# Optimization experiments

Hardware: AMD Instinct MI355X
Metric: run time of the kernel (lower is better)

The kernel has to match this reference:

```python
import jax, jax.numpy as jnp
import numpy as np

T = 2048
N = 4096
DT = 0.01
V_RESET = 1.0
ALPHA = 0.01
MAX_SPIKES = 128


def setup_inputs() -> dict:
    key = jax.random.key(0)
    ks = jax.random.split(key, 8)
    ts = jnp.arange(T, dtype=jnp.float32) * DT
    input_current = jax.random.normal(ks[0], (T, N), dtype=jnp.float32)
    # _build_w: uniform(minval=0.5) fully-connected weight matrix
    w = jax.random.uniform(ks[1], (N, N), dtype=jnp.float32, minval=0.5, maxval=1.0)
    # _build_initial: uniform(maxval=0.1)
    v0 = jax.random.uniform(ks[2], (N,), dtype=jnp.float32, maxval=0.1)
    i0 = jax.random.uniform(ks[3], (N,), dtype=jnp.float32, maxval=0.1)
    mu = jax.random.uniform(ks[4], (2,), dtype=jnp.float32, minval=0.5, maxval=1.0)
    # uniforms for initial s and for post-spike s resampling (s = log(u) - alpha)
    s0_u = jax.random.uniform(ks[5], (N,), dtype=jnp.float32)
    resample_u = jax.random.uniform(ks[6], (T, N), dtype=jnp.float32)
    return {"ts": ts, "input_current": input_current, "w": w, "v0": v0,
            "i0": i0, "mu": mu, "s0_u": s0_u, "resample_u": resample_u,
            "max_spikes": MAX_SPIKES}


def reference(ts, input_current, w, v0, i0, mu, s0_u, resample_u, max_spikes):
    """Event-driven spiking net: Euler integration of the drift vf with
    spike events when s crosses 0, followed by the masked per-neuron jump
    transition (_inner_trans_fn) using the firing neuron's weight row.
    Returns trajectory ys [T, N, 3] (v, i, s per neuron)."""
    dt = ts[1] - ts[0]
    eps = jnp.float32(1e-12)
    # s0 = log(uniform) - alpha  (always negative; drifts up at rate intensity(v))
    s0 = jnp.log(s0_u + eps) - ALPHA
    y0 = jnp.stack([v0, i0, s0], axis=-1)  # [N, 3]
    mu1, mu2 = mu[0], mu[1]

    def step(carry, xs):
        y, nsp = carry
        inp_t, ru_t = xs
        v, i, s = y[:, 0], y[:, 1], y[:, 2]
        # drift_vf (Euler step)
        v_n = v + dt * (mu1 * (i - v) + mu1 * inp_t)
        i_n = i + dt * (-mu2 * i)
        s_n = s + dt * jax.nn.sigmoid(v)  # intensity_fn(v)
        # event detection: cond_fn = s; event when s reaches 0
        ev = s_n >= 0.0  # [N] event mask
        fire = jnp.any(ev) & (nsp < max_spikes)
        idx = jnp.argmax(ev)  # event_idx = argmax over event mask
        w_row = w[idx]  # weights from firing neuron to all neurons
        # _inner_trans_fn: spiking neurons reset v and resample s;
        # non-spiking neurons receive current injection w[idx][j]
        v_t = jnp.where(ev, v_n - V_RESET, v_n)
        i_t = jnp.where(ev, i_n, i_n + w_row)
        s_t = jnp.where(ev, jnp.log(ru_t + eps) - ALPHA, s_n)
        y_fire = jnp.stack([v_t, i_t, s_t], axis=-1)
        y_free = jnp.stack([v_n, i_n, s_n], axis=-1)
        y_out = jnp.where(fire, y_fire, y_free)
        nsp = nsp + fire.astype(jnp.int32)
        return (y_out, nsp), y_out

    (_, _), ys = jax.lax.scan(step, (y0, jnp.int32(0)),
                              (input_current, resample_u))
    return ys
```

## Files before the change

### kernel.cpp

```cpp
#include <hip/hip_runtime.h>
#include <stddef.h>

#define TT 2048
#define NN 4096
#define LSEG 64
#define NSEG (TT / LSEG)
#define NBLK 16
#define TPA 64
#define NPT 4
#define TPB 256
#define WCAP 256
#define MAXU 0xFFFFFFFFu
#define NOFIRE 0xFFFFFFFEu

__global__ __launch_bounds__(TPA) void phaseA1(
    const float* __restrict__ ts, const float* __restrict__ inp,
    const float* __restrict__ w, const float* __restrict__ v0,
    const float* __restrict__ i0, const float* __restrict__ mu,
    const float* __restrict__ s0u, const float* __restrict__ ru,
    const int* __restrict__ mx, unsigned int* __restrict__ hdr,
    unsigned int* __restrict__ slots, unsigned int* __restrict__ fireT,
    unsigned int* __restrict__ fireIdx)
{
#pragma clang fp contract(off)
  const int tid = threadIdx.x;
  const int blk = blockIdx.x;
  const int idx4 = blk * TPA + tid;
  const int n0 = idx4 * NPT;
  const float dt = ts[1] - ts[0];
  const float mu1 = mu[0], mu2 = mu[1];
  const int maxs = mx[0];

  const float4* inp4 = (const float4*)inp;
  const float4* ru4  = (const float4*)ru;
  const float4* w4   = (const float4*)w;

  float4 a4;
  a4 = ((const float4*)v0)[idx4];  float v[NPT]    = {a4.x, a4.y, a4.z, a4.w};
  a4 = ((const float4*)i0)[idx4];  float i_nw[NPT] = {a4.x, a4.y, a4.z, a4.w};
  a4 = ((const float4*)s0u)[idx4];
  float s[NPT] = {logf(a4.x + 1e-12f) - 0.01f, logf(a4.y + 1e-12f) - 0.01f,
                  logf(a4.z + 1e-12f) - 0.01f, logf(a4.w + 1e-12f) - 0.01f};

  float snP[NPT] = {0.f, 0.f, 0.f, 0.f};
  bool  evP[NPT] = {false, false, false, false};
  bool  aw[NPT]  = {false, false, false, false};
  float wvP[NPT] = {0.f, 0.f, 0.f, 0.f};
  float4 inp_cur = make_float4(0.f,0.f,0.f,0.f);
  float4 ru_cur  = make_float4(0.f,0.f,0.f,0.f);
  int nsp = 0;
  int t_stop = TT;
  bool pubPrev = false;

  for (int t = 0;; ++t) {
    bool  fire2 = false;
    bool  awN[NPT] = {false, false, false, false};
    float wN[NPT]  = {0.f, 0.f, 0.f, 0.f};

    if (t >= 2) {
      unsigned int gm2 = NOFIRE;
      if (pubPrev) {
        const unsigned int* row = &slots[(size_t)(t - 2) * NBLK];
        unsigned int x = MAXU;
        long g = 0;
        for (;;) {
          x = __hip_atomic_load(&row[tid & (NBLK - 1)], __ATOMIC_RELAXED,
                                __HIP_MEMORY_SCOPE_AGENT);
          if (__ballot(x != MAXU) == ~0ULL) break;
          if (++g > (1L << 20)) break;
        }
        gm2 = x;
#pragma unroll
        for (int off = 1; off < NBLK; off <<= 1) {
          unsigned int o = (unsigned int)__shfl_xor((int)gm2, off, 64);
          gm2 = gm2 < o ? gm2 : o;
        }
      }
      fire2 = (gm2 < (unsigned int)NN) && (nsp < maxs);
      if (fire2) {
        if (blk == 0 && tid == 0 && nsp < WCAP) {
          fireT[nsp] = (unsigned int)(t - 2);
          fireIdx[nsp] = gm2;
        }
        float4 wr = w4[(size_t)gm2 * (NN / 4) + idx4];
        wN[0] = wr.x; wN[1] = wr.y; wN[2] = wr.z; wN[3] = wr.w;
#pragma unroll
        for (int k = 0; k < NPT; ++k) awN[k] = !evP[k];
        nsp += 1;
        if (nsp >= maxs) {
          t_stop = ((t - 1 + LSEG - 1) / LSEG) * LSEG;
          if (t_stop > TT) t_stop = TT;
          break;
        }
      }
      if (t - 1 == TT) { t_stop = TT; break; }
    }

    if (t >= 2) {
      float iv[NPT] = {inp_cur.x, inp_cur.y, inp_cur.z, inp_cur.w};
      float rv[NPT] = {ru_cur.x,  ru_cur.y,  ru_cur.z,  ru_cur.w};
#pragma unroll
      for (int k = 0; k < NPT; ++k) {
        float ifull = aw[k] ? (i_nw[k] + wvP[k]) : i_nw[k];
        float vn  = v[k] + dt * (mu1 * (ifull - v[k]) + mu1 * iv[k]);
        float in_ = ifull + dt * (-mu2 * ifull);
        if (evP[k] && fire2) {
          v[k] = vn - 1.0f;
          s[k] = logf(rv[k] + 1e-12f) - 0.01f;
        } else {
          v[k] = vn; s[k] = snP[k];
        }
        i_nw[k] = in_;
      }
    }

    bool pubNow = false;
    bool evN[NPT] = {false, false, false, false};
    if (t >= 1) {
      unsigned int m = NOFIRE;
#pragma unroll
      for (int k = 0; k < NPT; ++k) {
        float sig = 1.0f / (1.0f + expf(-v[k]));
        float sn = s[k] + dt * sig;
        snP[k] = sn;
        bool e = sn >= 0.0f;
        evN[k] = e;
        unsigned int c = e ? (unsigned int)(n0 + k) : NOFIRE;
        m = m < c ? m : c;
      }
#pragma unroll
      for (int off = 1; off < 64; off <<= 1) {
        unsigned int o = (unsigned int)__shfl_xor((int)m, off, 64);
        m = m < o ? m : o;
      }
      if (tid == 0)
        __hip_atomic_store(&slots[(size_t)(t - 1) * NBLK + blk], m,
                           __ATOMIC_RELAXED, __HIP_MEMORY_SCOPE_AGENT);
      pubNow = true;
    }

    float4 inw = make_float4(0.f,0.f,0.f,0.f);
    float4 rnw = make_float4(0.f,0.f,0.f,0.f);
    if (t >= 1 && t - 1 < TT) {
      inw = inp4[(size_t)(t - 1) * (NN / 4) + idx4];
      rnw = ru4[(size_t)(t - 1) * (NN / 4) + idx4];
    }

#pragma unroll
    for (int k = 0; k < NPT; ++k) {
      evP[k] = evN[k]; aw[k] = awN[k]; wvP[k] = wN[k];
    }
    inp_cur = inw; ru_cur = rnw;
    pubPrev = pubNow;
  }

  if (blk == 0 && tid == 0) {
    hdr[0] = (unsigned int)t_stop;
    hdr[1] = (unsigned int)nsp;
  }
}

__global__ __launch_bounds__(TPA) void phaseA2(
    const float* __restrict__ ts, const float* __restrict__ inp,
    const float* __restrict__ w, const float* __restrict__ v0,
    const float* __restrict__ i0, const float* __restrict__ mu,
    const float* __restrict__ s0u, const float* __restrict__ ru,
    const unsigned int* __restrict__ hdr, const unsigned int* __restrict__ fireT,
    const unsigned int* __restrict__ fireIdx, float* __restrict__ ys)
{
#pragma clang fp contract(off)
  const int tid = threadIdx.x;
  const int n = blockIdx.x * TPA + tid;
  const int Kp = (int)hdr[0];
  int nf = (int)hdr[1]; if (nf > WCAP) nf = WCAP;
  const float dt = ts[1] - ts[0];
  const float mu1 = mu[0], mu2 = mu[1];

  __shared__ unsigned int sT[WCAP];
  __shared__ float wlds[WCAP][TPA];
  for (int k = tid; k < nf; k += TPA) sT[k] = fireT[k];
  for (int k0 = 0; k0 < nf; k0 += 8) {
    float tmp[8];
#pragma unroll
    for (int j = 0; j < 8; ++j) {
      int k = k0 + j;
      tmp[j] = (k < nf) ? w[(size_t)fireIdx[k] * NN + n] : 0.0f;
    }
#pragma unroll
    for (int j = 0; j < 8; ++j) {
      int k = k0 + j;
      if (k < nf) wlds[k][tid] = tmp[j];
    }
  }
  __syncthreads();

  float v = v0[n];
  float i = i0[n];
  float s = logf(s0u[n] + 1e-12f) - 0.01f;

  float ib[8], rb[8];
#pragma unroll
  for (int j = 0; j < 8; ++j) {
    ib[j] = inp[(size_t)j * NN + n];
    rb[j] = ru[(size_t)j * NN + n];
  }
  int kp = 0;
  for (int tb = 0; tb < Kp; tb += 8) {
#pragma unroll
    for (int j = 0; j < 8; ++j) {
      const int t = tb + j;
      const float x   = ib[j];
      const float ruv = rb[j];
      if (t + 8 < Kp) {
        ib[j] = inp[(size_t)(t + 8) * NN + n];
        rb[j] = ru[(size_t)(t + 8) * NN + n];
      }
      float sig = 1.0f / (1.0f + expf(-v));
      float sn = s + dt * sig;
      bool e = sn >= 0.0f;
      float vn  = v + dt * (mu1 * (i - v) + mu1 * x);
      float in_ = i + dt * (-mu2 * i);
      bool fire = (kp < nf) && (sT[kp] == (unsigned int)t);
      if (fire) {
        float wc = wlds[kp][tid];
        ++kp;
        if (e) { v = vn - 1.0f; i = in_;      s = logf(ruv + 1e-12f) - 0.01f; }
        else   { v = vn;        i = in_ + wc; s = sn; }
      } else   { v = vn;        i = in_;      s = sn; }
      size_t o = ((size_t)t * NN + n) * 3;
      *(float3*)(ys + o) = make_float3(v, i, s);
    }
  }
}

__global__ __launch_bounds__(TPB) void p1_segc(
    const float* __restrict__ ts, const float* __restrict__ inp,
    const float* __restrict__ mu, const float* __restrict__ ys,
    const unsigned int* __restrict__ hdr, float* __restrict__ buf1)
{
  unsigned int Kp = hdr[0];
  unsigned int g0 = Kp / LSEG;
  unsigned int g = blockIdx.x >> 4;
  if (g < g0) return;
  int n = (blockIdx.x & 15) * TPB + threadIdx.x;
  float dt = ts[1] - ts[0];
  float mu1 = mu[0], mu2 = mu[1];
  float a = 1.0f - dt * mu1, b = dt * mu1, r = 1.0f - dt * mu2;
  float ibase = ys[((size_t)(Kp - 1) * NN + n) * 3 + 1];
  float ij = ibase * powf(r, (float)((int)(g * LSEG) - (int)Kp));
  float c = 0.0f;
  size_t base = (size_t)(g * LSEG) * NN + n;
  for (int j = 0; j < LSEG; ++j) {
    float x = inp[base + (size_t)j * NN];
    c = a * c + b * (ij + x);
    ij *= r;
  }
  buf1[(size_t)g * NN + n] = c;
}

__global__ __launch_bounds__(TPB) void p2_scanv(
    const float* __restrict__ ts, const float* __restrict__ mu,
    const float* __restrict__ ys, const unsigned int* __restrict__ hdr,
    float* __restrict__ buf1)
{
  unsigned int Kp = hdr[0];
  unsigned int g0 = Kp / LSEG;
  if (g0 >= NSEG) return;
  int n = blockIdx.x * TPB + threadIdx.x;
  float dt = ts[1] - ts[0];
  float mu1 = mu[0];
  float a = 1.0f - dt * mu1;
  float aL = a;
  for (int k = 0; k < 6; ++k) aL *= aL;
  float v = ys[((size_t)(Kp - 1) * NN + n) * 3 + 0];
  for (unsigned int g = g0; g < NSEG; ++g) {
    float cg = buf1[(size_t)g * NN + n];
    buf1[(size_t)g * NN + n] = v;
    v = aL * v + cg;
  }
}

__global__ __launch_bounds__(TPB) void p3_seg(
    const float* __restrict__ ts, const float* __restrict__ inp,
    const float* __restrict__ mu, const unsigned int* __restrict__ hdr,
    const float* __restrict__ buf1, float* __restrict__ buf2,
    float* __restrict__ ys)
{
  unsigned int Kp = hdr[0];
  unsigned int g0 = Kp / LSEG;
  unsigned int g = blockIdx.x >> 4;
  if (g < g0) return;
  int n = (blockIdx.x & 15) * TPB + threadIdx.x;
  float dt = ts[1] - ts[0];
  float mu1 = mu[0], mu2 = mu[1];
  float r = 1.0f - dt * mu2;
  float v = buf1[(size_t)g * NN + n];
  float ibase = ys[((size_t)(Kp - 1) * NN + n) * 3 + 1];
  float i = ibase * powf(r, (float)((int)(g * LSEG) - (int)Kp));
  float sl = 0.0f;
  for (int j = 0; j < LSEG; ++j) {
    size_t t = (size_t)g * LSEG + j;
    float x = inp[t * NN + n];
    float sig = 1.0f / (1.0f + expf(-v));
    sl = sl + dt * sig;
    float vn  = v + dt * (mu1 * (i - v) + mu1 * x);
    float in_ = i + dt * (-mu2 * i);
    size_t o = (t * NN + n) * 3;
    ys[o] = vn; ys[o + 1] = in_; ys[o + 2] = sl;
    v = vn; i = in_;
  }
  buf2[(size_t)g * NN + n] = sl;
}

__global__ __launch_bounds__(TPB) void p4_scans(
    const float* __restrict__ ys, const unsigned int* __restrict__ hdr,
    float* __restrict__ buf2)
{
  unsigned int Kp = hdr[0];
  unsigned int g0 = Kp / LSEG;
  if (g0 >= NSEG) return;
  int n = blockIdx.x * TPB + threadIdx.x;
  float s = ys[((size_t)(Kp - 1) * NN + n) * 3 + 2];
  for (unsigned int g = g0; g < NSEG; ++g) {
    float t = buf2[(size_t)g * NN + n];
    buf2[(size_t)g * NN + n] = s;
    s += t;
  }
}

__global__ __launch_bounds__(TPB) void p5_fixs(
    const unsigned int* __restrict__ hdr, const float* __restrict__ buf2,
    float* __restrict__ ys)
{
  unsigned int Kp = hdr[0];
  size_t e = (size_t)Kp * NN + (size_t)blockIdx.x * TPB + threadIdx.x;
  if (e >= (size_t)TT * NN) return;
  unsigned int t = (unsigned int)(e >> 12);
  unsigned int n = (unsigned int)(e & (NN - 1));
  unsigned int g = t >> 6;
  ys[e * 3 + 2] += buf2[(size_t)g * NN + n];
}

extern "C" void kernel_launch(void* const* d_in, const int* in_sizes, int n_in,
                              void* d_out, int out_size, void* d_ws, size_t ws_size,
                              hipStream_t stream)
{
  (void)in_sizes; (void)n_in; (void)out_size; (void)ws_size;
  const float* ts  = (const float*)d_in[0];
  const float* inp = (const float*)d_in[1];
  const float* w   = (const float*)d_in[2];
  const float* v0  = (const float*)d_in[3];
  const float* i0  = (const float*)d_in[4];
  const float* mu  = (const float*)d_in[5];
  const float* s0u = (const float*)d_in[6];
  const float* ru  = (const float*)d_in[7];
  const int*   mx  = (const int*)d_in[8];
  float* ys = (float*)d_out;

  char* wsb = (char*)d_ws;
  unsigned int* hdr     = (unsigned int*)wsb;
  unsigned int* fireT   = (unsigned int*)(wsb + 256);
  unsigned int* fireIdx = (unsigned int*)(wsb + 1280);
  unsigned int* slots   = (unsigned int*)(wsb + 4096);
  float* buf1 = (float*)(wsb + 4096 + (size_t)TT * NBLK * 4);
  float* buf2 = buf1 + (size_t)NSEG * NN;

  hipMemsetAsync(slots, 0xFF, (size_t)TT * NBLK * 4, stream);

  phaseA1<<<NBLK, TPA, 0, stream>>>(ts, inp, w, v0, i0, mu, s0u, ru, mx,
                                    hdr, slots, fireT, fireIdx);
  phaseA2<<<NN / TPA, TPA, 0, stream>>>(ts, inp, w, v0, i0, mu, s0u, ru,
                                        hdr, fireT, fireIdx, ys);
  p1_segc<<<NSEG * 16, TPB, 0, stream>>>(ts, inp, mu, ys, hdr, buf1);
  p2_scanv<<<NN / TPB, TPB, 0, stream>>>(ts, mu, ys, hdr, buf1);
  p3_seg<<<NSEG * 16, TPB, 0, stream>>>(ts, inp, mu, hdr, buf1, buf2, ys);
  p4_scans<<<NN / TPB, TPB, 0, stream>>>(ys, hdr, buf2);
  p5_fixs<<<(TT - 128) * NN / TPB, TPB, 0, stream>>>(hdr, buf2, ys);
}
```

Before: 654.9 us.

## Replace multi-block atomic spin sync with single 1024-thread block barrier

The sequential spike-detection phase moves from 16 single-wave blocks that synchronise each timestep through global atomic slots and spin-polling to one 1024-thread block. The per-step argmin is now exchanged through LDS with a workgroup barrier. The change also adds an 8-deep register ring prefetch of input currents and loads resample values only for neurons that fire. This removes the slot memset and the cross-CU latency, but puts the whole serial phase on a single CU.

```diff
diff --git a/kernel.cpp b/kernel.cpp
--- a/kernel.cpp
+++ b/kernel.cpp
@@ -5,159 +5,142 @@
 #define NN 4096
 #define LSEG 64
 #define NSEG (TT / LSEG)
-#define NBLK 16
+#define TPA1 1024
 #define TPA 64
 #define NPT 4
 #define TPB 256
 #define WCAP 256
+#define RING 8
 #define MAXU 0xFFFFFFFFu
 #define NOFIRE 0xFFFFFFFEu
 
-__global__ __launch_bounds__(TPA) void phaseA1(
+__global__ __launch_bounds__(TPA1) void phaseA(
     const float* __restrict__ ts, const float* __restrict__ inp,
     const float* __restrict__ w, const float* __restrict__ v0,
     const float* __restrict__ i0, const float* __restrict__ mu,
     const float* __restrict__ s0u, const float* __restrict__ ru,
     const int* __restrict__ mx, unsigned int* __restrict__ hdr,
-    unsigned int* __restrict__ slots, unsigned int* __restrict__ fireT,
-    unsigned int* __restrict__ fireIdx)
+    unsigned int* __restrict__ fireT, unsigned int* __restrict__ fireIdx)
 {
 #pragma clang fp contract(off)
   const int tid = threadIdx.x;
-  const int blk = blockIdx.x;
-  const int idx4 = blk * TPA + tid;
-  const int n0 = idx4 * NPT;
+  const int wid = tid >> 6;
+  const int lane = tid & 63;
+  const int n0 = tid * NPT;
   const float dt = ts[1] - ts[0];
   const float mu1 = mu[0], mu2 = mu[1];
   const int maxs = mx[0];
 
   const float4* inp4 = (const float4*)inp;
-  const float4* ru4  = (const float4*)ru;
   const float4* w4   = (const float4*)w;
 
   float4 a4;
-  a4 = ((const float4*)v0)[idx4];  float v[NPT]    = {a4.x, a4.y, a4.z, a4.w};
-  a4 = ((const float4*)i0)[idx4];  float i_nw[NPT] = {a4.x, a4.y, a4.z, a4.w};
-  a4 = ((const float4*)s0u)[idx4];
+  a4 = ((const float4*)v0)[tid];  float v[NPT]    = {a4.x, a4.y, a4.z, a4.w};
+  a4 = ((const float4*)i0)[tid];  float i_nw[NPT] = {a4.x, a4.y, a4.z, a4.w};
+  a4 = ((const float4*)s0u)[tid];
   float s[NPT] = {logf(a4.x + 1e-12f) - 0.01f, logf(a4.y + 1e-12f) - 0.01f,
                   logf(a4.z + 1e-12f) - 0.01f, logf(a4.w + 1e-12f) - 0.01f};
 
-  float snP[NPT] = {0.f, 0.f, 0.f, 0.f};
-  bool  evP[NPT] = {false, false, false, false};
-  bool  aw[NPT]  = {false, false, false, false};
-  float wvP[NPT] = {0.f, 0.f, 0.f, 0.f};
-  float4 inp_cur = make_float4(0.f,0.f,0.f,0.f);
-  float4 ru_cur  = make_float4(0.f,0.f,0.f,0.f);
+  float wv[NPT] = {0.f, 0.f, 0.f, 0.f};
+  bool  aw[NPT] = {false, false, false, false};
   int nsp = 0;
   int t_stop = TT;
-  bool pubPrev = false;
-
-  for (int t = 0;; ++t) {
-    bool  fire2 = false;
-    bool  awN[NPT] = {false, false, false, false};
-    float wN[NPT]  = {0.f, 0.f, 0.f, 0.f};
-
-    if (t >= 2) {
-      unsigned int gm2 = NOFIRE;
-      if (pubPrev) {
-        const unsigned int* row = &slots[(size_t)(t - 2) * NBLK];
-        unsigned int x = MAXU;
-        long g = 0;
-        for (;;) {
-          x = __hip_atomic_load(&row[tid & (NBLK - 1)], __ATOMIC_RELAXED,
-                                __HIP_MEMORY_SCOPE_AGENT);
-          if (__ballot(x != MAXU) == ~0ULL) break;
-          if (++g > (1L << 20)) break;
-        }
-        gm2 = x;
-#pragma unroll
-        for (int off = 1; off < NBLK; off <<= 1) {
-          unsigned int o = (unsigned int)__shfl_xor((int)gm2, off, 64);
-          gm2 = gm2 < o ? gm2 : o;
-        }
-      }
-      fire2 = (gm2 < (unsigned int)NN) && (nsp < maxs);
-      if (fire2) {
-        if (blk == 0 && tid == 0 && nsp < WCAP) {
-          fireT[nsp] = (unsigned int)(t - 2);
-          fireIdx[nsp] = gm2;
-        }
-        float4 wr = w4[(size_t)gm2 * (NN / 4) + idx4];
-        wN[0] = wr.x; wN[1] = wr.y; wN[2] = wr.z; wN[3] = wr.w;
-#pragma unroll
-        for (int k = 0; k < NPT; ++k) awN[k] = !evP[k];
-        nsp += 1;
-        if (nsp >= maxs) {
-          t_stop = ((t - 1 + LSEG - 1) / LSEG) * LSEG;
-          if (t_stop > TT) t_stop = TT;
-          break;
-        }
-      }
-      if (t - 1 == TT) { t_stop = TT; break; }
-    }
-
-    if (t >= 2) {
-      float iv[NPT] = {inp_cur.x, inp_cur.y, inp_cur.z, inp_cur.w};
-      float rv[NPT] = {ru_cur.x,  ru_cur.y,  ru_cur.z,  ru_cur.w};
+
+  __shared__ unsigned int shw[2][16];
+
+  float4 ib[RING];
+#pragma unroll
+  for (int j = 0; j < RING; ++j) ib[j] = inp4[(size_t)j * (NN / 4) + tid];
+
+  for (int tb = 0; tb < TT; tb += RING) {
+#pragma unroll
+    for (int j = 0; j < RING; ++j) {
+      const int t = tb + j;
+      const float4 cur = ib[j];
+      if (t + RING < TT)
+        ib[j] = inp4[(size_t)(t + RING) * (NN / 4) + tid];
+
+      float sn[NPT], rv[NPT];
+      bool ev[NPT];
+      unsigned int m = NOFIRE;
 #pragma unroll
       for (int k = 0; k < NPT; ++k) {
-        float ifull = aw[k] ? (i_nw[k] + wvP[k]) : i_nw[k];
+        float sig = 1.0f / (1.0f + expf(-v[k]));
+        sn[k] = s[k] + dt * sig;
+        ev[k] = sn[k] >= 0.0f;
+        unsigned int c = ev[k] ? (unsigned int)(n0 + k) : NOFIRE;
+        m = m < c ? m : c;
+        rv[k] = ev[k] ? ru[(size_t)t * NN + (n0 + k)] : 0.0f;
+      }
+
+#pragma unroll
+      for (int off = 32; off > 0; off >>= 1) {
+        unsigned int o = (unsigned int)__shfl_down((int)m, off, 64);
+        m = m < o ? m : o;
+      }
+      const int p = t & 1;
+      if (lane == 0) shw[p][wid] = m;
+      asm volatile("s_waitcnt lgkmcnt(0)" ::: "memory");
+      __builtin_amdgcn_sched_barrier(0);
+      __builtin_amdgcn_s_barrier();
+      __builtin_amdgcn_sched_barrier(0);
+
+      unsigned int gm;
+      {
+        const uint4* sp = (const uint4*)&shw[p][0];
+        uint4 q0 = sp[0], q1 = sp[1], q2 = sp[2], q3 = sp[3];
+        unsigned int m0 = q0.x < q0.y ? q0.x : q0.y;
+        unsigned int m1 = q0.z < q0.w ? q0.z : q0.w;
+        unsigned int m2 = q1.x < q1.y ? q1.x : q1.y;
+        unsigned int m3 = q1.z < q1.w ? q1.z : q1.w;
+        unsigned int m4 = q2.x < q2.y ? q2.x : q2.y;
+        unsigned int m5 = q2.z < q2.w ? q2.z : q2.w;
+        unsigned int m6 = q3.x < q3.y ? q3.x : q3.y;
+        unsigned int m7 = q3.z < q3.w ? q3.z : q3.w;
+        m0 = m0 < m1 ? m0 : m1;  m2 = m2 < m3 ? m2 : m3;
+        m4 = m4 < m5 ? m4 : m5;  m6 = m6 < m7 ? m6 : m7;
+        m0 = m0 < m2 ? m0 : m2;  m4 = m4 < m6 ? m4 : m6;
+        gm = m0 < m4 ? m0 : m4;
+      }
+      const bool fire = (gm < (unsigned int)NN) && (nsp < maxs);
+
+      float iv[NPT] = {cur.x, cur.y, cur.z, cur.w};
+#pragma unroll
+      for (int k = 0; k < NPT; ++k) {
+        float ifull = aw[k] ? (i_nw[k] + wv[k]) : i_nw[k];
         float vn  = v[k] + dt * (mu1 * (ifull - v[k]) + mu1 * iv[k]);
         float in_ = ifull + dt * (-mu2 * ifull);
-        if (evP[k] && fire2) {
-          v[k] = vn - 1.0f;
-          s[k] = logf(rv[k] + 1e-12f) - 0.01f;
+        if (fire) {
+          if (ev[k]) {
+            v[k] = vn - 1.0f;
+            s[k] = logf(rv[k] + 1e-12f) - 0.01f;
+            aw[k] = false;
+          } else {
+            v[k] = vn; s[k] = sn[k]; aw[k] = true;
+          }
         } else {
-          v[k] = vn; s[k] = snP[k];
+          v[k] = vn; s[k] = sn[k]; aw[k] = false;
         }
         i_nw[k] = in_;
       }
+      if (fire) {
+        float4 wr = w4[(size_t)gm * (NN / 4) + tid];
+        wv[0] = wr.x; wv[1] = wr.y; wv[2] = wr.z; wv[3] = wr.w;
+        if (tid == 0 && nsp < WCAP) {
+          fireT[nsp] = (unsigned int)t;
+          fireIdx[nsp] = gm;
+        }
+        ++nsp;
+        if (nsp >= maxs) {
+          t_stop = ((t + 1 + LSEG - 1) >> 6) << 6;
+          if (t_stop > TT) t_stop = TT;
+          goto done;
+        }
+      }
     }
-
-    bool pubNow = false;
-    bool evN[NPT] = {false, false, false, false};
-    if (t >= 1) {
-      unsigned int m = NOFIRE;
-#pragma unroll
-      for (int k = 0; k < NPT; ++k) {
-        float sig = 1.0f / (1.0f + expf(-v[k]));
-        float sn = s[k] + dt * sig;
-        snP[k] = sn;
-        bool e = sn >= 0.0f;
-        evN[k] = e;
-        unsigned int c = e ? (unsigned int)(n0 + k) : NOFIRE;
-        m = m < c ? m : c;
-      }
-#pragma unroll
-      for (int off = 1; off < 64; off <<= 1) {
-        unsigned int o = (unsigned int)__shfl_xor((int)m, off, 64);
-        m = m < o ? m : o;
-      }
-      if (tid == 0)
-        __hip_atomic_store(&slots[(size_t)(t - 1) * NBLK + blk], m,
-                           __ATOMIC_RELAXED, __HIP_MEMORY_SCOPE_AGENT);
-      pubNow = true;
-    }
-
-    float4 inw = make_float4(0.f,0.f,0.f,0.f);
-    float4 rnw = make_float4(0.f,0.f,0.f,0.f);
-    if (t >= 1 && t - 1 < TT) {
-      inw = inp4[(size_t)(t - 1) * (NN / 4) + idx4];
-      rnw = ru4[(size_t)(t - 1) * (NN / 4) + idx4];
-    }
-
-#pragma unroll
-    for (int k = 0; k < NPT; ++k) {
-      evP[k] = evN[k]; aw[k] = awN[k]; wvP[k] = wN[k];
-    }
-    inp_cur = inw; ru_cur = rnw;
-    pubPrev = pubNow;
-  }
-
-  if (blk == 0 && tid == 0) {
-    hdr[0] = (unsigned int)t_stop;
-    hdr[1] = (unsigned int)nsp;
-  }
+  }
+done:
+  if (tid == 0) { hdr[0] = (unsigned int)t_stop; hdr[1] = (unsigned int)nsp; }
 }
 
 __global__ __launch_bounds__(TPA) void phaseA2(
@@ -361,14 +344,11 @@
   unsigned int* hdr     = (unsigned int*)wsb;
   unsigned int* fireT   = (unsigned int*)(wsb + 256);
   unsigned int* fireIdx = (unsigned int*)(wsb + 1280);
-  unsigned int* slots   = (unsigned int*)(wsb + 4096);
-  float* buf1 = (float*)(wsb + 4096 + (size_t)TT * NBLK * 4);
+  float* buf1 = (float*)(wsb + 4096);
   float* buf2 = buf1 + (size_t)NSEG * NN;
 
-  hipMemsetAsync(slots, 0xFF, (size_t)TT * NBLK * 4, stream);
-
-  phaseA1<<<NBLK, TPA, 0, stream>>>(ts, inp, w, v0, i0, mu, s0u, ru, mx,
-                                    hdr, slots, fireT, fireIdx);
+  phaseA<<<1, TPA1, 0, stream>>>(ts, inp, w, v0, i0, mu, s0u, ru, mx,
+                                 hdr, fireT, fireIdx);
   phaseA2<<<NN / TPA, TPA, 0, stream>>>(ts, inp, w, v0, i0, mu, s0u, ru,
                                         hdr, fireT, fireIdx, ys);
   p1_segc<<<NSEG * 16, TPB, 0, stream>>>(ts, inp, mu, ys, hdr, buf1);
```

Result: slower. 766.9 us (+17.1%).
